# Kernel tuning notes

Hardware: AMD Instinct MI355X
Metric: run time of the kernel (lower is better)

Reference implementation:

```python
import jax, jax.numpy as jnp
import numpy as np

EPS = 1e-3  # Keras LayerNormalization default epsilon


def layernorm(x, g, b):
    mu = jnp.mean(x, axis=-1, keepdims=True)
    var = jnp.var(x, axis=-1, keepdims=True)
    return (x - mu) * jax.lax.rsqrt(var + EPS) * g + b


def setup_inputs() -> dict:
    key = jax.random.key(0)
    ks = jax.random.split(key, 16)
    B, T, C = 2, 2048, 1024
    F = 4 * C
    std = 0.02
    inp = {
        "x": jax.random.normal(ks[0], (B, T, C), jnp.float32),
        "ln1_g": jnp.ones((C,), jnp.float32),
        "ln1_b": jnp.zeros((C,), jnp.float32),
        "Wq": std * jax.random.normal(ks[1], (C, C), jnp.float32),
        "bq": jnp.zeros((C,), jnp.float32),
        "Wk": std * jax.random.normal(ks[2], (C, C), jnp.float32),
        "bk": jnp.zeros((C,), jnp.float32),
        "Wv": std * jax.random.normal(ks[3], (C, C), jnp.float32),
        "bv": jnp.zeros((C,), jnp.float32),
        "ln2_g": jnp.ones((C,), jnp.float32),
        "ln2_b": jnp.zeros((C,), jnp.float32),
        "W1": std * jax.random.normal(ks[4], (C, F), jnp.float32),
        "b1": jnp.zeros((F,), jnp.float32),
        "W2": std * jax.random.normal(ks[5], (F, C), jnp.float32),
        "b2": jnp.zeros((C,), jnp.float32),
    }
    return inp


N_HEADS = 16


def reference(x, ln1_g, ln1_b, Wq, bq, Wk, bk, Wv, bv, ln2_g, ln2_b, W1, b1, W2, b2):
    B, T, C = x.shape
    H = N_HEADS
    D = C // H

    h = layernorm(x, ln1_g, ln1_b)
    # [B,T,C] -> [B,H,T,D]
    def split_heads(y):
        return y.reshape(B, T, H, D).transpose(0, 2, 1, 3)

    q = split_heads(h @ Wq + bq)
    k = split_heads(h @ Wk + bk)
    v = split_heads(h @ Wv + bv)

    # Faithful to original: scores = K @ Q^T, i.e. scores[i,j] = k_i . q_j
    scores = jnp.einsum("bhid,bhjd->bhij", k, q) / jnp.sqrt(jnp.float32(D))
    causal = jnp.tril(jnp.ones((T, T), bool))  # [T,T]
    scores = jnp.where(causal[None, None], scores, -jnp.inf)
    w = jax.nn.softmax(scores, axis=-1)
    attn = jnp.einsum("bhij,bhjd->bhid", w, v)  # [B,H,T,D]
    attn = attn.transpose(0, 2, 1, 3).reshape(B, T, C)
    x = x + attn

    h2 = layernorm(x, ln2_g, ln2_b)
    ffn = jax.nn.gelu(h2 @ W1 + b1, approximate=False) @ W2 + b2
    x = x + ffn
    return x
```

## Files before the change

### kernel.cpp

```cpp
#include <hip/hip_runtime.h>
#include <hip/hip_bf16.h>
#include <math.h>

typedef __hip_bfloat16 bf16;
typedef __attribute__((ext_vector_type(8))) short bf16x8;
typedef __attribute__((ext_vector_type(4))) float f32x4;

__device__ __forceinline__ unsigned short f2bf_rne(float f) {
  unsigned u = __float_as_uint(f);
  u += 0x7fffu + ((u >> 16) & 1u);
  return (unsigned short)(u >> 16);
}
__device__ __forceinline__ float bf2f(unsigned short s) {
  return __uint_as_float(((unsigned)s) << 16);
}

__device__ __forceinline__ float gelu_fast(float v) {
  float u = v * (0.7978845608f + 0.0356774081f * v * v);
  float t = __builtin_amdgcn_exp2f(u * 2.8853900818f);
  float r = __builtin_amdgcn_rcpf(t + 1.0f);
  return v - v * r;
}

#define GLOBAL_AS __attribute__((address_space(1)))
#define LDS_AS __attribute__((address_space(3)))
__device__ __forceinline__ void gl2lds16(const void* g, void* l) {
  __builtin_amdgcn_global_load_lds((const GLOBAL_AS void*)g, (LDS_AS void*)l, 16, 0, 0);
}

__global__ __launch_bounds__(256) void ln_kernel(const float* __restrict__ x,
                                                 const float* __restrict__ g,
                                                 const float* __restrict__ b,
                                                 bf16* __restrict__ h) {
  int row = blockIdx.x, t = threadIdx.x;
  const float4 xv = ((const float4*)(x + (size_t)row * 1024))[t];
  float s = xv.x + xv.y + xv.z + xv.w;
  float sq = xv.x * xv.x + xv.y * xv.y + xv.z * xv.z + xv.w * xv.w;
  #pragma unroll
  for (int m = 1; m < 64; m <<= 1) { s += __shfl_xor(s, m); sq += __shfl_xor(sq, m); }
  __shared__ float ps[4], pq[4];
  if ((t & 63) == 0) { ps[t >> 6] = s; pq[t >> 6] = sq; }
  __syncthreads();
  s = ps[0] + ps[1] + ps[2] + ps[3];
  sq = pq[0] + pq[1] + pq[2] + pq[3];
  float mean = s * (1.0f / 1024.0f);
  float var = sq * (1.0f / 1024.0f) - mean * mean;
  float rs = rsqrtf(var + 1e-3f);
  float4 gv = ((const float4*)g)[t];
  float4 bv = ((const float4*)b)[t];
  ushort4 o;
  o.x = f2bf_rne((xv.x - mean) * rs * gv.x + bv.x);
  o.y = f2bf_rne((xv.y - mean) * rs * gv.y + bv.y);
  o.z = f2bf_rne((xv.z - mean) * rs * gv.z + bv.z);
  o.w = f2bf_rne((xv.w - mean) * rs * gv.w + bv.w);
  ((ushort4*)(h + (size_t)row * 1024))[t] = o;
}

__device__ __forceinline__ void tr_tile(const float* __restrict__ W, bf16* __restrict__ WT,
                                        int R, int Cc, int bx, int by, int t) {
  __shared__ float tile[32][33];
  int tx = t & 31, ty = t >> 5;
  #pragma unroll
  for (int k = 0; k < 4; k++) {
    int rr = ty + k * 8;
    tile[rr][tx] = W[(size_t)(by + rr) * Cc + bx + tx];
  }
  __syncthreads();
  unsigned short* out = reinterpret_cast<unsigned short*>(WT);
  #pragma unroll
  for (int k = 0; k < 4; k++) {
    int rr = ty + k * 8;
    out[(size_t)(bx + rr) * R + by + tx] = f2bf_rne(tile[tx][rr]);
  }
}

__global__ __launch_bounds__(256) void transpose_all(const float* __restrict__ Wq,
                                                     const float* __restrict__ Wk,
                                                     const float* __restrict__ Wv,
                                                     const float* __restrict__ W1,
                                                     const float* __restrict__ W2,
                                                     bf16* __restrict__ WqkT,
                                                     bf16* __restrict__ W1T,
                                                     bf16* __restrict__ W2T) {
  int id = blockIdx.x, t = threadIdx.x;
  if (id < 3072) {
    int sect = id >> 10, r = id & 1023;
    const float* W = sect == 0 ? Wq : (sect == 1 ? Wk : Wv);
    bf16* WT = WqkT + (size_t)sect * 1048576;
    tr_tile(W, WT, 1024, 1024, (r & 31) * 32, (r >> 5) * 32, t);
  } else if (id < 7168) {
    int r = id - 3072;
    tr_tile(W1, W1T, 1024, 4096, (r & 127) * 32, (r >> 7) * 32, t);
  } else {
    int r = id - 7168;
    tr_tile(W2, W2T, 4096, 1024, (r & 31) * 32, (r >> 5) * 32, t);
  }
}

__device__ __forceinline__ void mainloop_256(const bf16* __restrict__ A,
                                             const bf16* __restrict__ BT,
                                             int K, int m0, int n0,
                                             char* ldsb, int t,
                                             f32x4 (&acc)[8][4]) {
  const int lane = t & 63, wave = t >> 6;
  const int l = lane & 15, quad = lane >> 4;
  const int wm = (wave >> 2) * 128, wn = (wave & 3) * 64;
  const int srow = wave * 8 + (lane >> 3);
  const int scol = ((lane & 7) ^ (lane >> 3)) * 8;
  const int grp0 = (quad ^ (l & 7)) * 16;
  const int grp1 = ((4 + quad) ^ (l & 7)) * 16;

  bf16x8 a[4][2], b01[2][2], b23[2][2];

  auto stA = [&](int buf, int half, int kt) {
    const bf16* s = A + (size_t)(m0 + half * 128 + srow) * K + kt * 64 + scol;
    char* d = ldsb + buf * 65536 + half * 16384 + wave * 1024;
    gl2lds16(s, d);
    gl2lds16(s + (size_t)64 * K, d + 8192);
  };
  auto stB = [&](int buf, int half, int kt) {
    const bf16* s = BT + (size_t)(n0 + half * 128 + srow) * K + kt * 64 + scol;
    char* d = ldsb + buf * 65536 + 32768 + half * 16384 + wave * 1024;
    gl2lds16(s, d);
    gl2lds16(s + (size_t)64 * K, d + 8192);
  };
  auto rdA = [&](int buf, int mh) {
    const char* base = ldsb + buf * 65536 + (wm + mh * 64 + l) * 128;
    #pragma unroll
    for (int ii = 0; ii < 4; ii++) {
      a[ii][0] = *(const bf16x8*)(base + ii * 2048 + grp0);
      a[ii][1] = *(const bf16x8*)(base + ii * 2048 + grp1);
    }
  };
  auto rdB = [&](int buf, int nh, bf16x8 (&bb)[2][2]) {
    const char* base = ldsb + buf * 65536 + 32768 + (wn + nh * 32 + l) * 128;
    #pragma unroll
    for (int jj = 0; jj < 2; jj++) {
      bb[jj][0] = *(const bf16x8*)(base + jj * 2048 + grp0);
      bb[jj][1] = *(const bf16x8*)(base + jj * 2048 + grp1);
    }
  };
  auto mm4 = [&](int mi, bf16x8 (&bb)[2][2], int nj) {
    #pragma unroll
    for (int ii = 0; ii < 4; ii++)
      #pragma unroll
      for (int jj = 0; jj < 2; jj++) {
        acc[mi + ii][nj + jj] = __builtin_amdgcn_mfma_f32_16x16x32_bf16(
            a[ii][0], bb[jj][0], acc[mi + ii][nj + jj], 0, 0, 0);
        acc[mi + ii][nj + jj] = __builtin_amdgcn_mfma_f32_16x16x32_bf16(
            a[ii][1], bb[jj][1], acc[mi + ii][nj + jj], 0, 0, 0);
      }
  };

#define BARX() __builtin_amdgcn_s_barrier()
#define LGKM0() do { asm volatile("s_waitcnt lgkmcnt(0)" ::: "memory"); \
                     __builtin_amdgcn_sched_barrier(0); } while (0)
#define HALF4(BC, DOA, SAB, SAK, DOB, SBB, SBK, VMN)                      \
  do {                                                                    \
    rdA(BC, 0); rdB(BC, 0, b01);                                          \
    if (DOA) stA(SAB, 0, SAK);                                            \
    BARX(); LGKM0();                                                      \
    __builtin_amdgcn_s_setprio(1); mm4(0, b01, 0);                        \
    __builtin_amdgcn_s_setprio(0); BARX();                                \
    rdB(BC, 1, b23);                                                      \
    if (DOA) stA(SAB, 1, SAK);                                            \
    BARX(); LGKM0();                                                      \
    __builtin_amdgcn_s_setprio(1); mm4(0, b23, 2);                        \
    __builtin_amdgcn_s_setprio(0); BARX();                                \
    rdA(BC, 1);                                                           \
    if (DOB) stB(SBB, 0, SBK);                                            \
    BARX(); LGKM0();                                                      \
    __builtin_amdgcn_s_setprio(1); mm4(4, b01, 0);                        \
    __builtin_amdgcn_s_setprio(0); BARX();                                \
    if (DOB) stB(SBB, 1, SBK);                                            \
    BARX();                                                               \
    __builtin_amdgcn_s_setprio(1); mm4(4, b23, 2);                        \
    __builtin_amdgcn_s_setprio(0);                                        \
    asm volatile("s_waitcnt vmcnt(" VMN ")" ::: "memory");                \
    BARX();                                                               \
  } while (0)

  const int nt = K >> 6;
  stA(0, 0, 0); stA(0, 1, 0);
  stB(0, 0, 0); stB(0, 1, 0);
  stB(1, 0, 1); stB(1, 1, 1);
  asm volatile("s_waitcnt vmcnt(4)" ::: "memory");
  BARX();
  int tt = 0;
  for (; tt + 2 < nt; tt += 2) {
    HALF4(0, 1, 1, tt + 1, 1, 0, tt + 2, "4");
    HALF4(1, 1, 0, tt + 2, 1, 1, tt + 3, "4");
  }
  HALF4(0, 1, 1, tt + 1, 0, 0, 0, "0");
  HALF4(1, 0, 0, 0, 0, 0, 0, "0");
#undef HALF4
#undef LGKM0
#undef BARX
}

__global__ __launch_bounds__(512, 2) void gemm_ffn1(const bf16* __restrict__ A,
                                                    const bf16* __restrict__ BT,
                                                    const float* __restrict__ bias,
                                                    bf16* __restrict__ out,
                                                    int N, int K) {
  extern __shared__ char lds[];
  int t = threadIdx.x;
  int n0 = blockIdx.x * 256, m0 = blockIdx.y * 256;
  f32x4 acc[8][4];
  #pragma unroll
  for (int i = 0; i < 8; i++)
    #pragma unroll
    for (int j = 0; j < 4; j++) acc[i][j] = (f32x4){0.f, 0.f, 0.f, 0.f};
  mainloop_256(A, BT, K, m0, n0, lds, t, acc);

  int lane = t & 63, wave = t >> 6;
  int l = lane & 15, quad = lane >> 4;
  int wm = (wave >> 2) * 128, wn = (wave & 3) * 64;
  int r4 = quad * 4;
  unsigned short* os = reinterpret_cast<unsigned short*>(out);
  #pragma unroll
  for (int i = 0; i < 8; i++)
    #pragma unroll
    for (int j = 0; j < 4; j++) {
      int col = n0 + wn + j * 16 + l;
      float bval = bias[col];
      #pragma unroll
      for (int r = 0; r < 4; r++) {
        int row = m0 + wm + i * 16 + r4 + r;
        os[(size_t)row * N + col] = f2bf_rne(gelu_fast(acc[i][j][r] + bval));
      }
    }
}

__global__ __launch_bounds__(512, 2) void gemm_qkv(const bf16* __restrict__ A,
                                                   const bf16* __restrict__ BT,
                                                   const float* __restrict__ bq,
                                                   const float* __restrict__ bk,
                                                   const float* __restrict__ bv,
                                                   bf16* __restrict__ qb,
                                                   bf16* __restrict__ kb,
                                                   bf16* __restrict__ vt,
                                                   int K) {
  extern __shared__ char lds[];
  int t = threadIdx.x;
  int n0 = blockIdx.x * 256, m0 = blockIdx.y * 256;
  f32x4 acc[8][4];
  #pragma unroll
  for (int i = 0; i < 8; i++)
    #pragma unroll
    for (int j = 0; j < 4; j++) acc[i][j] = (f32x4){0.f, 0.f, 0.f, 0.f};
  mainloop_256(A, BT, K, m0, n0, lds, t, acc);

  int lane = t & 63, wave = t >> 6;
  int l = lane & 15, quad = lane >> 4;
  int wm = (wave >> 2) * 128, wn = (wave & 3) * 64;
  int sect = n0 >> 10;
  const float* bias = sect == 0 ? bq : (sect == 1 ? bk : bv);
  int r4 = quad * 4;
  #pragma unroll
  for (int i = 0; i < 8; i++)
    #pragma unroll
    for (int j = 0; j < 4; j++) {
      int col = n0 + wn + j * 16 + l;
      int c1 = col & 1023;
      float bval = bias[c1];
      int row0 = m0 + wm + i * 16 + r4;
      if (sect < 2) {
        bf16* o = sect == 0 ? qb : kb;
        unsigned short* os = reinterpret_cast<unsigned short*>(o);
        #pragma unroll
        for (int r = 0; r < 4; r++)
          os[(size_t)(row0 + r) * 1024 + c1] = f2bf_rne(acc[i][j][r] + bval);
      } else {
        int hh = c1 >> 6, d = c1 & 63;
        int b = row0 >> 11, t0 = row0 & 2047;
        ushort4 pk;
        pk.x = f2bf_rne(acc[i][j][0] + bval);
        pk.y = f2bf_rne(acc[i][j][1] + bval);
        pk.z = f2bf_rne(acc[i][j][2] + bval);
        pk.w = f2bf_rne(acc[i][j][3] + bval);
        *(ushort4*)((unsigned short*)vt + (size_t)((b * 16 + hh) * 64 + d) * 2048 + t0) = pk;
      }
    }
}

__device__ __forceinline__ void kloop_bk64(const bf16* __restrict__ A,
                                           const bf16* __restrict__ BT,
                                           int K, int kbeg, int kend, int m0, int n0,
                                           int wave, int lane,
                                           bf16 (*As)[64], bf16 (*Bs)[64],
                                           f32x4 acc[4][4]) {
  int lrow = lane & 15, quad = lane >> 4;
  int wm = (wave >> 1) * 64, wn = (wave & 1) * 64;
  int srow = wave * 32 + (lane >> 3);
  int gsw = ((lane & 7) ^ (lane >> 3)) * 8;
  int sw = lrow & 7;
  for (int k0 = kbeg; k0 < kend; k0 += 64) {
    __syncthreads();
    #pragma unroll
    for (int j = 0; j < 4; j++) {
      int row = srow + j * 8;
      gl2lds16(A + (size_t)(m0 + row) * K + k0 + gsw, (char*)As + wave * 4096 + j * 1024);
      gl2lds16(BT + (size_t)(n0 + row) * K + k0 + gsw, (char*)Bs + wave * 4096 + j * 1024);
    }
    __syncthreads();
    bf16x8 af[2][4], bfr[2][4];
    #pragma unroll
    for (int h = 0; h < 2; h++) {
      #pragma unroll
      for (int i = 0; i < 4; i++)
        af[h][i] = *(const bf16x8*)((const char*)&As[wm + i * 16 + lrow][0] +
                                    (((h * 4 + quad) ^ sw) * 16));
      #pragma unroll
      for (int j = 0; j < 4; j++)
        bfr[h][j] = *(const bf16x8*)((const char*)&Bs[wn + j * 16 + lrow][0] +
                                     (((h * 4 + quad) ^ sw) * 16));
    }
    #pragma unroll
    for (int h = 0; h < 2; h++)
      #pragma unroll
      for (int i = 0; i < 4; i++)
        #pragma unroll
        for (int j = 0; j < 4; j++)
          acc[i][j] = __builtin_amdgcn_mfma_f32_16x16x32_bf16(af[h][i], bfr[h][j], acc[i][j], 0, 0, 0);
  }
}

__global__ __launch_bounds__(256) void gemm_ffn2_sk(const bf16* __restrict__ A,
                                                    const bf16* __restrict__ BT,
                                                    unsigned short* __restrict__ p0,
                                                    unsigned short* __restrict__ p1,
                                                    int K) {
  __shared__ bf16 As[128][64];
  __shared__ bf16 Bs[128][64];
  int t = threadIdx.x;
  int n0 = blockIdx.x * 128, m0 = blockIdx.y * 128;
  int z = blockIdx.z;
  int lane = t & 63, wave = t >> 6;
  f32x4 acc[4][4];
  #pragma unroll
  for (int i = 0; i < 4; i++)
    #pragma unroll
    for (int j = 0; j < 4; j++) acc[i][j] = (f32x4){0.f, 0.f, 0.f, 0.f};
  kloop_bk64(A, BT, K, z * 2048, z * 2048 + 2048, m0, n0, wave, lane, As, Bs, acc);

  unsigned short* p = z ? p1 : p0;
  int wm = (wave >> 1) * 64, wn = (wave & 1) * 64;
  int r4 = (lane >> 4) * 4, cl = lane & 15;
  #pragma unroll
  for (int i = 0; i < 4; i++)
    #pragma unroll
    for (int j = 0; j < 4; j++) {
      int col = n0 + wn + j * 16 + cl;
      #pragma unroll
      for (int r = 0; r < 4; r++) {
        int row = m0 + wm + i * 16 + r4 + r;
        p[(size_t)row * 1024 + col] = f2bf_rne(acc[i][j][r]);
      }
    }
}

__global__ __launch_bounds__(256) void reduce_ffn2(const unsigned short* __restrict__ p0,
                                                   const unsigned short* __restrict__ p1,
                                                   const float* __restrict__ x1,
                                                   const float* __restrict__ bias,
                                                   float* __restrict__ out) {
  int row = blockIdx.x, t = threadIdx.x;
  size_t base = (size_t)row * 1024;
  ushort4 a = ((const ushort4*)(p0 + base))[t];
  ushort4 b = ((const ushort4*)(p1 + base))[t];
  float4 xv = ((const float4*)(x1 + base))[t];
  float4 bv = ((const float4*)bias)[t];
  float4 o;
  o.x = bf2f(a.x) + bf2f(b.x) + xv.x + bv.x;
  o.y = bf2f(a.y) + bf2f(b.y) + xv.y + bv.y;
  o.z = bf2f(a.z) + bf2f(b.z) + xv.z + bv.z;
  o.w = bf2f(a.w) + bf2f(b.w) + xv.w + bv.w;
  ((float4*)(out + base))[t] = o;
}

__global__ __launch_bounds__(256) void attn_mfma(const bf16* __restrict__ qb,
                                                 const bf16* __restrict__ kb,
                                                 const bf16* __restrict__ vt,
                                                 const float* __restrict__ x,
                                                 float* __restrict__ x1) {
  __shared__ bf16 QP[64][72];
  __shared__ bf16 KV[2][2][64][64];
  int t = threadIdx.x;
  int bh = blockIdx.x;
  int b = bh >> 4, h = bh & 15;
  size_t qk_base = (size_t)b * 2048 * 1024 + (size_t)h * 64;
  size_t vt_base = (size_t)bh * 64 * 2048;
  int lane = t & 63, wave = t >> 6;
  int l = lane & 15, quad = lane >> 4;
  int sw = l & 7;
  int srow8 = lane >> 3;
  int scol = ((lane & 7) ^ srow8) * 8;
  const float cs = 0.125f * 1.44269504088896f;
  int y = blockIdx.y;

  for (int pass = 0; pass < 2; pass++) {
    int it = pass ? 31 - y : y;
    int i0 = it * 64;
    int njt = it + 1;
    __syncthreads();
    #pragma unroll
    for (int c0 = 0; c0 < 512; c0 += 256) {
      int c = c0 + t;
      int row = c >> 3, col8 = (c & 7) * 8;
      *(uint4*)&QP[row][col8] = *(const uint4*)(kb + qk_base + (size_t)(i0 + row) * 1024 + col8);
    }
    #pragma unroll
    for (int c = 0; c < 2; c++) {
      int rr = wave * 16 + c * 8 + srow8;
      gl2lds16(qb + qk_base + (size_t)rr * 1024 + scol,
               (char*)KV + wave * 2048 + c * 1024);
      gl2lds16(vt + vt_base + (size_t)rr * 2048 + scol,
               (char*)KV + 8192 + wave * 2048 + c * 1024);
    }
    __syncthreads();

    bf16x8 qf0 = *(const bf16x8*)&QP[wave * 16 + l][quad * 8];
    bf16x8 qf1 = *(const bf16x8*)&QP[wave * 16 + l][32 + quad * 8];
    float lsum = 0.f;
    f32x4 Oacc[4];
    #pragma unroll
    for (int dt = 0; dt < 4; dt++) Oacc[dt] = (f32x4){0.f, 0.f, 0.f, 0.f};
    int iblk = i0 + wave * 16;

    int buf = 0;
    for (int jt = 0; jt < njt; jt++) {
      int j0v = jt * 64;
      if (jt + 1 < njt) {
        int j1 = j0v + 64;
        #pragma unroll
        for (int c = 0; c < 2; c++) {
          int rr = wave * 16 + c * 8 + srow8;
          gl2lds16(qb + qk_base + (size_t)(j1 + rr) * 1024 + scol,
                   (char*)KV + (buf ^ 1) * 16384 + wave * 2048 + c * 1024);
          gl2lds16(vt + vt_base + (size_t)rr * 2048 + j1 + scol,
                   (char*)KV + (buf ^ 1) * 16384 + 8192 + wave * 2048 + c * 1024);
        }
      }

      const bf16* Kb = &KV[buf][0][0][0];
      #pragma unroll
      for (int nt = 0; nt < 4; nt++) {
        int jb = j0v + nt * 16;
        uint2 pk;
        if (jb > iblk + 15) {
          pk.x = 0u; pk.y = 0u;
        } else {
          const bf16* kr = Kb + (nt * 16 + l) * 64;
          bf16x8 kf0 = *(const bf16x8*)(kr + ((quad ^ sw) * 8));
          bf16x8 kf1 = *(const bf16x8*)(kr + (((4 + quad) ^ sw) * 8));
          f32x4 sv = (f32x4){0.f, 0.f, 0.f, 0.f};
          sv = __builtin_amdgcn_mfma_f32_16x16x32_bf16(kf0, qf0, sv, 0, 0, 0);
          sv = __builtin_amdgcn_mfma_f32_16x16x32_bf16(kf1, qf1, sv, 0, 0, 0);
          float p0, p1, p2, p3;
          if (jb + 15 <= iblk) {
            p0 = __builtin_amdgcn_exp2f(sv[0] * cs);
            p1 = __builtin_amdgcn_exp2f(sv[1] * cs);
            p2 = __builtin_amdgcn_exp2f(sv[2] * cs);
            p3 = __builtin_amdgcn_exp2f(sv[3] * cs);
          } else {
            int i_ = iblk + l, jbase = jb + quad * 4;
            p0 = (jbase + 0 > i_) ? 0.f : __builtin_amdgcn_exp2f(sv[0] * cs);
            p1 = (jbase + 1 > i_) ? 0.f : __builtin_amdgcn_exp2f(sv[1] * cs);
            p2 = (jbase + 2 > i_) ? 0.f : __builtin_amdgcn_exp2f(sv[2] * cs);
            p3 = (jbase + 3 > i_) ? 0.f : __builtin_amdgcn_exp2f(sv[3] * cs);
          }
          lsum += (p0 + p1) + (p2 + p3);
          union { __hip_bfloat162 h2; unsigned u; } c0u, c1u;
          c0u.h2 = __float22bfloat162_rn(make_float2(p0, p1));
          c1u.h2 = __float22bfloat162_rn(make_float2(p2, p3));
          pk.x = c0u.u; pk.y = c1u.u;
        }
        *(uint2*)&QP[wave * 16 + l][nt * 16 + quad * 4] = pk;
      }
      asm volatile("s_waitcnt lgkmcnt(0)" ::: "memory");

      bf16x8 ap0 = *(const bf16x8*)&QP[wave * 16 + l][quad * 8];
      bf16x8 ap1 = *(const bf16x8*)&QP[wave * 16 + l][32 + quad * 8];
      const bf16* Vb = &KV[buf][1][0][0];
      #pragma unroll
      for (int dt = 0; dt < 4; dt++) {
        const bf16* vr = Vb + (dt * 16 + l) * 64;
        bf16x8 bv0 = *(const bf16x8*)(vr + ((quad ^ sw) * 8));
        bf16x8 bv1 = *(const bf16x8*)(vr + (((4 + quad) ^ sw) * 8));
        Oacc[dt] = __builtin_amdgcn_mfma_f32_16x16x32_bf16(ap0, bv0, Oacc[dt], 0, 0, 0);
        Oacc[dt] = __builtin_amdgcn_mfma_f32_16x16x32_bf16(ap1, bv1, Oacc[dt], 0, 0, 0);
      }
      __syncthreads();
      buf ^= 1;
    }

    lsum += __shfl_xor(lsum, 16);
    lsum += __shfl_xor(lsum, 32);
    #pragma unroll
    for (int r = 0; r < 4; r++) {
      float lv = __shfl(lsum, quad * 4 + r);
      float inv = 1.0f / lv;
      int row = i0 + wave * 16 + quad * 4 + r;
      size_t gi = qk_base + (size_t)row * 1024;
      #pragma unroll
      for (int dt = 0; dt < 4; dt++) {
        int d = dt * 16 + l;
        x1[gi + d] = x[gi + d] + Oacc[dt][r] * inv;
      }
    }
  }
}

extern "C" void kernel_launch(void* const* d_in, const int* in_sizes, int n_in,
                              void* d_out, int out_size, void* d_ws, size_t ws_size,
                              hipStream_t stream) {
  const float* x    = (const float*)d_in[0];
  const float* ln1g = (const float*)d_in[1];
  const float* ln1b = (const float*)d_in[2];
  const float* Wq   = (const float*)d_in[3];
  const float* bq   = (const float*)d_in[4];
  const float* Wk   = (const float*)d_in[5];
  const float* bk   = (const float*)d_in[6];
  const float* Wv   = (const float*)d_in[7];
  const float* bv   = (const float*)d_in[8];
  const float* ln2g = (const float*)d_in[9];
  const float* ln2b = (const float*)d_in[10];
  const float* W1   = (const float*)d_in[11];
  const float* b1   = (const float*)d_in[12];
  const float* W2   = (const float*)d_in[13];
  const float* b2   = (const float*)d_in[14];

  char* ws = (char*)d_ws;
  float* x1  = (float*)(ws + 0);
  bf16* h    = (bf16*)(ws + 16777216);
  bf16* WqkT = (bf16*)(ws + 25165824);
  bf16* W1T  = (bf16*)(ws + 31457280);
  bf16* W2T  = (bf16*)(ws + 39845888);
  bf16* qb   = (bf16*)(ws + 48234496);
  bf16* kb   = (bf16*)(ws + 56623104);
  bf16* vt   = (bf16*)(ws + 65011712);
  bf16* act  = (bf16*)(ws + 73400320);

  static bool s_attr_done = false;
  if (!s_attr_done) {
    hipFuncSetAttribute(reinterpret_cast<const void*>(gemm_qkv),
                        hipFuncAttributeMaxDynamicSharedMemorySize, 131072);
    hipFuncSetAttribute(reinterpret_cast<const void*>(gemm_ffn1),
                        hipFuncAttributeMaxDynamicSharedMemorySize, 131072);
    s_attr_done = true;
  }

  transpose_all<<<11264, 256, 0, stream>>>(Wq, Wk, Wv, W1, W2, WqkT, W1T, W2T);
  ln_kernel<<<4096, 256, 0, stream>>>(x, ln1g, ln1b, h);
  gemm_qkv<<<dim3(12, 16), 512, 131072, stream>>>(h, WqkT, bq, bk, bv, qb, kb, vt, 1024);
  attn_mfma<<<dim3(32, 16), 256, 0, stream>>>(qb, kb, vt, x, x1);
  ln_kernel<<<4096, 256, 0, stream>>>(x1, ln2g, ln2b, h);
  gemm_ffn1<<<dim3(16, 16), 512, 131072, stream>>>(h, W1T, b1, act, 4096, 1024);
  gemm_ffn2_sk<<<dim3(8, 32, 2), 256, 0, stream>>>(act, W2T,
      (unsigned short*)qb, (unsigned short*)kb, 4096);
  reduce_ffn2<<<4096, 256, 0, stream>>>((const unsigned short*)qb, (const unsigned short*)kb,
                                        x1, b2, (float*)d_out);
}
```

Before: 304.2 us.

## Run FFN2 on the pipelined 256x256 GEMM mainloop with 4-way split-K

Replaces the simple 128x128 split-K=2 FFN2 GEMM with the double-buffered 256x256 mainloop used by the other GEMMs. The mainloop now takes separate row stride and K-extent arguments, and the K dimension is split four ways. The four bf16 partial outputs go into reused workspace buffers (qb, kb, vt, h) and a widened reduce kernel sums them. The aim is better data reuse and MFMA pipelining in the largest-K GEMM. In exchange it writes and reads twice as many bf16 partial buffers, and launches only 256 blocks of 512 threads.

```diff
diff --git a/kernel.cpp b/kernel.cpp
--- a/kernel.cpp
+++ b/kernel.cpp
@@ -99,7 +99,7 @@
 
 __device__ __forceinline__ void mainloop_256(const bf16* __restrict__ A,
                                              const bf16* __restrict__ BT,
-                                             int K, int m0, int n0,
+                                             int lda, int nk, int m0, int n0,
                                              char* ldsb, int t,
                                              f32x4 (&acc)[8][4]) {
   const int lane = t & 63, wave = t >> 6;
@@ -113,16 +113,16 @@
   bf16x8 a[4][2], b01[2][2], b23[2][2];
 
   auto stA = [&](int buf, int half, int kt) {
-    const bf16* s = A + (size_t)(m0 + half * 128 + srow) * K + kt * 64 + scol;
+    const bf16* s = A + (size_t)(m0 + half * 128 + srow) * lda + kt * 64 + scol;
     char* d = ldsb + buf * 65536 + half * 16384 + wave * 1024;
     gl2lds16(s, d);
-    gl2lds16(s + (size_t)64 * K, d + 8192);
+    gl2lds16(s + (size_t)64 * lda, d + 8192);
   };
   auto stB = [&](int buf, int half, int kt) {
-    const bf16* s = BT + (size_t)(n0 + half * 128 + srow) * K + kt * 64 + scol;
+    const bf16* s = BT + (size_t)(n0 + half * 128 + srow) * lda + kt * 64 + scol;
     char* d = ldsb + buf * 65536 + 32768 + half * 16384 + wave * 1024;
     gl2lds16(s, d);
-    gl2lds16(s + (size_t)64 * K, d + 8192);
+    gl2lds16(s + (size_t)64 * lda, d + 8192);
   };
   auto rdA = [&](int buf, int mh) {
     const char* base = ldsb + buf * 65536 + (wm + mh * 64 + l) * 128;
@@ -180,7 +180,7 @@
     BARX();                                                               \
   } while (0)
 
-  const int nt = K >> 6;
+  const int nt = nk >> 6;
   stA(0, 0, 0); stA(0, 1, 0);
   stB(0, 0, 0); stB(0, 1, 0);
   stB(1, 0, 1); stB(1, 1, 1);
@@ -211,7 +211,7 @@
   for (int i = 0; i < 8; i++)
     #pragma unroll
     for (int j = 0; j < 4; j++) acc[i][j] = (f32x4){0.f, 0.f, 0.f, 0.f};
-  mainloop_256(A, BT, K, m0, n0, lds, t, acc);
+  mainloop_256(A, BT, K, K, m0, n0, lds, t, acc);
 
   int lane = t & 63, wave = t >> 6;
   int l = lane & 15, quad = lane >> 4;
@@ -230,6 +230,64 @@
         os[(size_t)row * N + col] = f2bf_rne(gelu_fast(acc[i][j][r] + bval));
       }
     }
+}
+
+__global__ __launch_bounds__(512, 2) void gemm_ffn2(const bf16* __restrict__ A,
+                                                    const bf16* __restrict__ BT,
+                                                    unsigned short* __restrict__ p0,
+                                                    unsigned short* __restrict__ p1,
+                                                    unsigned short* __restrict__ p2,
+                                                    unsigned short* __restrict__ p3) {
+  extern __shared__ char lds[];
+  int t = threadIdx.x;
+  int n0 = blockIdx.x * 256, m0 = blockIdx.y * 256;
+  int z = blockIdx.z;
+  f32x4 acc[8][4];
+  #pragma unroll
+  for (int i = 0; i < 8; i++)
+    #pragma unroll
+    for (int j = 0; j < 4; j++) acc[i][j] = (f32x4){0.f, 0.f, 0.f, 0.f};
+  mainloop_256(A + z * 1024, BT + z * 1024, 4096, 1024, m0, n0, lds, t, acc);
+
+  unsigned short* p = z == 0 ? p0 : (z == 1 ? p1 : (z == 2 ? p2 : p3));
+  int lane = t & 63, wave = t >> 6;
+  int l = lane & 15, quad = lane >> 4;
+  int wm = (wave >> 2) * 128, wn = (wave & 3) * 64;
+  int r4 = quad * 4;
+  #pragma unroll
+  for (int i = 0; i < 8; i++)
+    #pragma unroll
+    for (int j = 0; j < 4; j++) {
+      int col = n0 + wn + j * 16 + l;
+      #pragma unroll
+      for (int r = 0; r < 4; r++) {
+        int row = m0 + wm + i * 16 + r4 + r;
+        p[(size_t)row * 1024 + col] = f2bf_rne(acc[i][j][r]);
+      }
+    }
+}
+
+__global__ __launch_bounds__(256) void reduce_ffn2(const unsigned short* __restrict__ p0,
+                                                   const unsigned short* __restrict__ p1,
+                                                   const unsigned short* __restrict__ p2,
+                                                   const unsigned short* __restrict__ p3,
+                                                   const float* __restrict__ x1,
+                                                   const float* __restrict__ bias,
+                                                   float* __restrict__ out) {
+  int row = blockIdx.x, t = threadIdx.x;
+  size_t base = (size_t)row * 1024;
+  ushort4 a = ((const ushort4*)(p0 + base))[t];
+  ushort4 b = ((const ushort4*)(p1 + base))[t];
+  ushort4 c = ((const ushort4*)(p2 + base))[t];
+  ushort4 d = ((const ushort4*)(p3 + base))[t];
+  float4 xv = ((const float4*)(x1 + base))[t];
+  float4 bv = ((const float4*)bias)[t];
+  float4 o;
+  o.x = (bf2f(a.x) + bf2f(b.x)) + (bf2f(c.x) + bf2f(d.x)) + xv.x + bv.x;
+  o.y = (bf2f(a.y) + bf2f(b.y)) + (bf2f(c.y) + bf2f(d.y)) + xv.y + bv.y;
+  o.z = (bf2f(a.z) + bf2f(b.z)) + (bf2f(c.z) + bf2f(d.z)) + xv.z + bv.z;
+  o.w = (bf2f(a.w) + bf2f(b.w)) + (bf2f(c.w) + bf2f(d.w)) + xv.w + bv.w;
+  ((float4*)(out + base))[t] = o;
 }
 
 __global__ __launch_bounds__(512, 2) void gemm_qkv(const bf16* __restrict__ A,
@@ -249,7 +307,7 @@
   for (int i = 0; i < 8; i++)
     #pragma unroll
     for (int j = 0; j < 4; j++) acc[i][j] = (f32x4){0.f, 0.f, 0.f, 0.f};
-  mainloop_256(A, BT, K, m0, n0, lds, t, acc);
+  mainloop_256(A, BT, K, K, m0, n0, lds, t, acc);
 
   int lane = t & 63, wave = t >> 6;
   int l = lane & 15, quad = lane >> 4;
@@ -282,101 +340,6 @@
         *(ushort4*)((unsigned short*)vt + (size_t)((b * 16 + hh) * 64 + d) * 2048 + t0) = pk;
       }
     }
-}
-
-__device__ __forceinline__ void kloop_bk64(const bf16* __restrict__ A,
-                                           const bf16* __restrict__ BT,
-                                           int K, int kbeg, int kend, int m0, int n0,
-                                           int wave, int lane,
-                                           bf16 (*As)[64], bf16 (*Bs)[64],
-                                           f32x4 acc[4][4]) {
-  int lrow = lane & 15, quad = lane >> 4;
-  int wm = (wave >> 1) * 64, wn = (wave & 1) * 64;
-  int srow = wave * 32 + (lane >> 3);
-  int gsw = ((lane & 7) ^ (lane >> 3)) * 8;
-  int sw = lrow & 7;
-  for (int k0 = kbeg; k0 < kend; k0 += 64) {
-    __syncthreads();
-    #pragma unroll
-    for (int j = 0; j < 4; j++) {
-      int row = srow + j * 8;
-      gl2lds16(A + (size_t)(m0 + row) * K + k0 + gsw, (char*)As + wave * 4096 + j * 1024);
-      gl2lds16(BT + (size_t)(n0 + row) * K + k0 + gsw, (char*)Bs + wave * 4096 + j * 1024);
-    }
-    __syncthreads();
-    bf16x8 af[2][4], bfr[2][4];
-    #pragma unroll
-    for (int h = 0; h < 2; h++) {
-      #pragma unroll
-      for (int i = 0; i < 4; i++)
-        af[h][i] = *(const bf16x8*)((const char*)&As[wm + i * 16 + lrow][0] +
-                                    (((h * 4 + quad) ^ sw) * 16));
-      #pragma unroll
-      for (int j = 0; j < 4; j++)
-        bfr[h][j] = *(const bf16x8*)((const char*)&Bs[wn + j * 16 + lrow][0] +
-                                     (((h * 4 + quad) ^ sw) * 16));
-    }
-    #pragma unroll
-    for (int h = 0; h < 2; h++)
-      #pragma unroll
-      for (int i = 0; i < 4; i++)
-        #pragma unroll
-        for (int j = 0; j < 4; j++)
-          acc[i][j] = __builtin_amdgcn_mfma_f32_16x16x32_bf16(af[h][i], bfr[h][j], acc[i][j], 0, 0, 0);
-  }
-}
-
-__global__ __launch_bounds__(256) void gemm_ffn2_sk(const bf16* __restrict__ A,
-                                                    const bf16* __restrict__ BT,
-                                                    unsigned short* __restrict__ p0,
-                                                    unsigned short* __restrict__ p1,
-                                                    int K) {
-  __shared__ bf16 As[128][64];
-  __shared__ bf16 Bs[128][64];
-  int t = threadIdx.x;
-  int n0 = blockIdx.x * 128, m0 = blockIdx.y * 128;
-  int z = blockIdx.z;
-  int lane = t & 63, wave = t >> 6;
-  f32x4 acc[4][4];
-  #pragma unroll
-  for (int i = 0; i < 4; i++)
-    #pragma unroll
-    for (int j = 0; j < 4; j++) acc[i][j] = (f32x4){0.f, 0.f, 0.f, 0.f};
-  kloop_bk64(A, BT, K, z * 2048, z * 2048 + 2048, m0, n0, wave, lane, As, Bs, acc);
-
-  unsigned short* p = z ? p1 : p0;
-  int wm = (wave >> 1) * 64, wn = (wave & 1) * 64;
-  int r4 = (lane >> 4) * 4, cl = lane & 15;
-  #pragma unroll
-  for (int i = 0; i < 4; i++)
-    #pragma unroll
-    for (int j = 0; j < 4; j++) {
-      int col = n0 + wn + j * 16 + cl;
-      #pragma unroll
-      for (int r = 0; r < 4; r++) {
-        int row = m0 + wm + i * 16 + r4 + r;
-        p[(size_t)row * 1024 + col] = f2bf_rne(acc[i][j][r]);
-      }
-    }
-}
-
-__global__ __launch_bounds__(256) void reduce_ffn2(const unsigned short* __restrict__ p0,
-                                                   const unsigned short* __restrict__ p1,
-                                                   const float* __restrict__ x1,
-                                                   const float* __restrict__ bias,
-                                                   float* __restrict__ out) {
-  int row = blockIdx.x, t = threadIdx.x;
-  size_t base = (size_t)row * 1024;
-  ushort4 a = ((const ushort4*)(p0 + base))[t];
-  ushort4 b = ((const ushort4*)(p1 + base))[t];
-  float4 xv = ((const float4*)(x1 + base))[t];
-  float4 bv = ((const float4*)bias)[t];
-  float4 o;
-  o.x = bf2f(a.x) + bf2f(b.x) + xv.x + bv.x;
-  o.y = bf2f(a.y) + bf2f(b.y) + xv.y + bv.y;
-  o.z = bf2f(a.z) + bf2f(b.z) + xv.z + bv.z;
-  o.w = bf2f(a.w) + bf2f(b.w) + xv.w + bv.w;
-  ((float4*)(out + base))[t] = o;
 }
 
 __global__ __launch_bounds__(256) void attn_mfma(const bf16* __restrict__ qb,
@@ -548,6 +511,8 @@
                         hipFuncAttributeMaxDynamicSharedMemorySize, 131072);
     hipFuncSetAttribute(reinterpret_cast<const void*>(gemm_ffn1),
                         hipFuncAttributeMaxDynamicSharedMemorySize, 131072);
+    hipFuncSetAttribute(reinterpret_cast<const void*>(gemm_ffn2),
+                        hipFuncAttributeMaxDynamicSharedMemorySize, 131072);
     s_attr_done = true;
   }
 
@@ -557,8 +522,9 @@
   attn_mfma<<<dim3(32, 16), 256, 0, stream>>>(qb, kb, vt, x, x1);
   ln_kernel<<<4096, 256, 0, stream>>>(x1, ln2g, ln2b, h);
   gemm_ffn1<<<dim3(16, 16), 512, 131072, stream>>>(h, W1T, b1, act, 4096, 1024);
-  gemm_ffn2_sk<<<dim3(8, 32, 2), 256, 0, stream>>>(act, W2T,
-      (unsigned short*)qb, (unsigned short*)kb, 4096);
+  gemm_ffn2<<<dim3(4, 16, 4), 512, 131072, stream>>>(act, W2T,
+      (unsigned short*)qb, (unsigned short*)kb, (unsigned short*)vt, (unsigned short*)h);
   reduce_ffn2<<<4096, 256, 0, stream>>>((const unsigned short*)qb, (const unsigned short*)kb,
+                                        (const unsigned short*)vt, (const unsigned short*)h,
                                         x1, b2, (float*)d_out);
 }
```

Result: faster. 291.4 us (-4.2%).
